# Optimization experiments

Hardware: AMD Instinct MI355X
Metric: run time of the kernel (lower is better)

## Reference

```python
import jax, jax.numpy as jnp
import numpy as np

EPS = 1e-7


def squash(s):
    # safe norm over last axis, keepdims
    norm = jnp.sqrt(jnp.sum(jnp.square(s), axis=-1, keepdims=True) + EPS)
    norm_sq = jnp.square(norm)
    return norm_sq / (1.0 + norm_sq) / norm * s


def setup_inputs() -> dict:
    key = jax.random.key(0)
    k1, k2 = jax.random.split(key)
    B, IN_CAPS, IN_DIM = 64, 2048, 16
    N_CAPS, CAP_DIM = 64, 16
    x = jax.random.normal(k1, (B, IN_CAPS, IN_DIM), dtype=jnp.float32)
    # glorot-uniform-ish init for W
    limit = (6.0 / (IN_DIM + N_CAPS * CAP_DIM)) ** 0.5
    W = jax.random.uniform(k2, (IN_CAPS, IN_DIM, N_CAPS * CAP_DIM),
                           minval=-limit, maxval=limit, dtype=jnp.float32)
    bias = jnp.zeros((N_CAPS, CAP_DIM), dtype=jnp.float32)
    return {"x": x, "W": W, "bias": bias}


def reference(x, W, bias):
    B, in_caps, in_dim = x.shape
    n_caps, cap_dim = bias.shape
    r_iters = 3
    # projection: [B, in_caps, n_caps*cap_dim] -> [B, in_caps, n_caps, cap_dim]
    u_hat = jnp.einsum('bij,ijk->bik', x, W).reshape(B, in_caps, n_caps, cap_dim)
    b = jnp.zeros((B, in_caps, n_caps, 1), dtype=u_hat.dtype)
    v = None
    for r in range(r_iters):
        c = jax.nn.softmax(b, axis=2)                       # route over class caps
        s = jnp.sum(u_hat * c, axis=1, keepdims=True)       # [B, 1, n_caps, cap_dim]
        s = s + bias
        v = squash(s)
        if r < r_iters - 1:
            agreement = jnp.sum(u_hat * v, axis=-1, keepdims=True)
            b = b + agreement
    return jnp.squeeze(v, axis=1)                           # [B, n_caps, cap_dim]
```

## Files before the change

### kernel.cpp

```cpp
#include <hip/hip_runtime.h>
#include <hip/hip_bf16.h>
#include <hip/hip_fp16.h>
#include <cstdio>

#define B_  64
#define I_  2048
#define J_  16
#define N_  64
#define D_  16
#define K_  1024

using short8 = __attribute__((ext_vector_type(8))) short;
using f32x16 = __attribute__((ext_vector_type(16))) float;

#if __has_builtin(__builtin_amdgcn_cvt_pk_u8_f32)
#define CVTPK_U8(f, sel, old) (unsigned)__builtin_amdgcn_cvt_pk_u8_f32((f), (sel), (old))
#else
__device__ __forceinline__ unsigned cvtpk_u8_sw(float f, unsigned sel, unsigned old) {
  unsigned b = (unsigned)(int)f & 0xffu;
  unsigned sh = sel * 8u;
  return (old & ~(0xffu << sh)) | (b << sh);
}
#define CVTPK_U8(f, sel, old) cvtpk_u8_sw((f), (sel), (old))
#endif

__device__ __forceinline__ short8 pack_bf16x8(float a0, float a1, float a2, float a3,
                                              float a4, float a5, float a6, float a7) {
  __hip_bfloat162 p0 = __float22bfloat162_rn(float2{a0, a1});
  __hip_bfloat162 p1 = __float22bfloat162_rn(float2{a2, a3});
  __hip_bfloat162 p2 = __float22bfloat162_rn(float2{a4, a5});
  __hip_bfloat162 p3 = __float22bfloat162_rn(float2{a6, a7});
  union { unsigned u[4]; short8 s; } cv;
  cv.u[0] = *(unsigned*)&p0; cv.u[1] = *(unsigned*)&p1;
  cv.u[2] = *(unsigned*)&p2; cv.u[3] = *(unsigned*)&p3;
  return cv.s;
}

__global__ __launch_bounds__(256, 5) void project_k(const float* __restrict__ x,
                                                    const float* __restrict__ W,
                                                    unsigned char* __restrict__ uh,
                                                    unsigned short* __restrict__ sc,
                                                    float* __restrict__ s_zero) {
  const int i  = blockIdx.x >> 2;
  const int ph = blockIdx.x & 3;
  const int t  = threadIdx.x;
  const int l  = t & 63;
  const int wv = t >> 6;
  const int h  = l >> 5;
  const int lr = l & 31;

  __shared__ unsigned       out_lds[64 * 65];
  __shared__ unsigned short sc_lds[64 * 20];

  if (blockIdx.x < 768) s_zero[blockIdx.x * 256 + t] = 0.f;

  short8 xfrag[2];
#pragma unroll
  for (int bt = 0; bt < 2; ++bt) {
    const float* xp = x + ((size_t)(bt * 32 + lr) * I_ + i) * J_ + h * 8;
    float4 f0 = *(const float4*)xp;
    float4 f1 = *(const float4*)(xp + 4);
    xfrag[bt] = pack_bf16x8(f0.x, f0.y, f0.z, f0.w, f1.x, f1.y, f1.z, f1.w);
  }

  const float* wbase = W + (size_t)i * (J_ * K_) + ph * 256;

#pragma unroll
  for (int kx = 0; kx < 2; ++kx) {
    const int kt = wv * 2 + kx;
    float wf[8];
#pragma unroll
    for (int e = 0; e < 8; ++e)
      wf[e] = wbase[(size_t)(h * 8 + e) * K_ + kt * 32 + lr];
    short8 afrag = pack_bf16x8(wf[0], wf[1], wf[2], wf[3], wf[4], wf[5], wf[6], wf[7]);

#pragma unroll
    for (int bt = 0; bt < 2; ++bt) {
      f32x16 acc = {0.f, 0.f, 0.f, 0.f, 0.f, 0.f, 0.f, 0.f,
                    0.f, 0.f, 0.f, 0.f, 0.f, 0.f, 0.f, 0.f};
      acc = __builtin_amdgcn_mfma_f32_32x32x16_bf16(afrag, xfrag[bt], acc, 0, 0, 0);
      const int b = bt * 32 + lr;

#define QCAP(C8, CS) do {                                                       \
      float ax = fabsf(acc[(C8) + 0]);                                          \
      ax = fmaxf(ax, fabsf(acc[(C8) + 1]));                                     \
      ax = fmaxf(ax, fabsf(acc[(C8) + 2]));                                     \
      ax = fmaxf(ax, fabsf(acc[(C8) + 3]));                                     \
      ax = fmaxf(ax, fabsf(acc[(C8) + 4]));                                     \
      ax = fmaxf(ax, fabsf(acc[(C8) + 5]));                                     \
      ax = fmaxf(ax, fabsf(acc[(C8) + 6]));                                     \
      ax = fmaxf(ax, fabsf(acc[(C8) + 7]));                                     \
      ax = fmaxf(ax, __shfl_xor(ax, 32));                                       \
      float inv = __fdividef(127.0f, fmaxf(ax, 1e-30f));                        \
      unsigned pk0 = CVTPK_U8(rintf(fmaf(acc[(C8) + 0], inv, 128.f)), 0u, 0u);  \
      pk0 = CVTPK_U8(rintf(fmaf(acc[(C8) + 1], inv, 128.f)), 1u, pk0);          \
      pk0 = CVTPK_U8(rintf(fmaf(acc[(C8) + 2], inv, 128.f)), 2u, pk0);          \
      pk0 = CVTPK_U8(rintf(fmaf(acc[(C8) + 3], inv, 128.f)), 3u, pk0);          \
      unsigned pk1 = CVTPK_U8(rintf(fmaf(acc[(C8) + 4], inv, 128.f)), 0u, 0u);  \
      pk1 = CVTPK_U8(rintf(fmaf(acc[(C8) + 5], inv, 128.f)), 1u, pk1);          \
      pk1 = CVTPK_U8(rintf(fmaf(acc[(C8) + 6], inv, 128.f)), 2u, pk1);          \
      pk1 = CVTPK_U8(rintf(fmaf(acc[(C8) + 7], inv, 128.f)), 3u, pk1);          \
      const int ibase = kt * 8 + (CS) * 4;                                      \
      out_lds[b * 65 + ibase + h]     = pk0;                                    \
      out_lds[b * 65 + ibase + 2 + h] = pk1;                                    \
      if (h == 0)                                                               \
        sc_lds[b * 20 + kt * 2 + (CS)] =                                        \
            __half_as_ushort(__float2half_rn(ax * (1.0f / 127.0f)));            \
    } while (0)

      QCAP(0, 0);
      QCAP(8, 1);
#undef QCAP
    }
  }
  __syncthreads();

  {
    const int c = t & 15;
#pragma unroll
    for (int it = 0; it < 4; ++it) {
      int bf = (t >> 4) + it * 16;
      const unsigned* rp = &out_lds[bf * 65 + c * 4];
      uint4 v;
      v.x = rp[0]; v.y = rp[1]; v.z = rp[2]; v.w = rp[3];
      *(uint4*)(uh + (size_t)bf * I_ * K_ + (size_t)i * K_ + ph * 256 + c * 16) = v;
    }
    int b2 = t >> 2, n4 = (t & 3) * 4;
    uint2 sv = *(const uint2*)&sc_lds[b2 * 20 + n4];
    *(uint2*)(sc + (size_t)b2 * I_ * N_ + (size_t)i * N_ + ph * 16 + n4) = sv;
  }
}

template <int MODE>
__global__ __launch_bounds__(256, 4) void route_k(const unsigned char* __restrict__ uh,
                                                  const unsigned short* __restrict__ sc,
                                                  const float* __restrict__ sa,
                                                  const float* __restrict__ sb,
                                                  const float* __restrict__ bias,
                                                  float* __restrict__ s_out) {
  const int t    = threadIdx.x;
  const int lane = t & 63;
  const int wv   = t >> 6;
  const int b    = blockIdx.x >> 4;
  const int iw   = ((blockIdx.x & 15) << 2) + wv;
  const int i0   = iw * 32;

  float vsum[16];
  float voff = 0.f;
  if (MODE >= 1) {
    float bs[16];
#pragma unroll
    for (int q = 0; q < 4; ++q) {
      float4 bb4 = *(const float4*)&bias[lane * 16 + q * 4];
      bs[q*4+0] = bb4.x; bs[q*4+1] = bb4.y; bs[q*4+2] = bb4.z; bs[q*4+3] = bb4.w;
    }
    {
      float va[16], nn = 0.f;
#pragma unroll
      for (int q = 0; q < 4; ++q) {
        float4 tmp = *(const float4*)&sa[(size_t)b * K_ + lane * 16 + q * 4];
        va[q*4+0] = tmp.x + bs[q*4+0]; va[q*4+1] = tmp.y + bs[q*4+1];
        va[q*4+2] = tmp.z + bs[q*4+2]; va[q*4+3] = tmp.w + bs[q*4+3];
      }
#pragma unroll
      for (int d = 0; d < 16; ++d) nn += va[d] * va[d];
      float n2 = nn + 1e-7f;
      float f = sqrtf(n2) / (1.0f + n2);
#pragma unroll
      for (int d = 0; d < 16; ++d) vsum[d] = va[d] * f;
    }
    if (MODE == 2) {
      float vb[16], nn = 0.f;
#pragma unroll
      for (int q = 0; q < 4; ++q) {
        float4 tmp = *(const float4*)&sb[(size_t)b * K_ + lane * 16 + q * 4];
        vb[q*4+0] = tmp.x + bs[q*4+0]; vb[q*4+1] = tmp.y + bs[q*4+1];
        vb[q*4+2] = tmp.z + bs[q*4+2]; vb[q*4+3] = tmp.w + bs[q*4+3];
      }
#pragma unroll
      for (int d = 0; d < 16; ++d) nn += vb[d] * vb[d];
      float n2 = nn + 1e-7f;
      float f = sqrtf(n2) / (1.0f + n2);
#pragma unroll
      for (int d = 0; d < 16; ++d) vsum[d] += vb[d] * f;
    }
    float tv = 0.f;
#pragma unroll
    for (int d = 0; d < 16; ++d) tv += vsum[d];
    voff = 128.0f * tv;
  }

  constexpr int IPW = 32;
  constexpr int PF  = 4;

  const unsigned char*  base = uh + (size_t)b * I_ * K_ + lane * 16;
  const unsigned short* scb  = sc + (size_t)b * I_ * N_ + lane;

  uint4 dbuf[PF];
  unsigned short hbuf[PF];
#pragma unroll
  for (int p = 0; p < PF; ++p) {
    int ip = (i0 + p) & (I_ - 1);
    dbuf[p] = *(const uint4*)(base + (size_t)ip * K_);
    hbuf[p] = scb[(size_t)ip * N_];
  }

  float s_loc[16];
#pragma unroll
  for (int d = 0; d < 16; ++d) s_loc[d] = 0.f;
  float csum = 0.f;

  for (int ii = 0; ii < IPW; ii += PF) {
#pragma unroll
    for (int p = 0; p < PF; ++p) {
      float scale = __half2float(__ushort_as_half(hbuf[p]));
      float u[16];
      {
        unsigned wd;
        wd = dbuf[p].x;
        u[0]  = (float)(wd & 0xffu);         u[1]  = (float)((wd >> 8) & 0xffu);
        u[2]  = (float)((wd >> 16) & 0xffu); u[3]  = (float)(wd >> 24);
        wd = dbuf[p].y;
        u[4]  = (float)(wd & 0xffu);         u[5]  = (float)((wd >> 8) & 0xffu);
        u[6]  = (float)((wd >> 16) & 0xffu); u[7]  = (float)(wd >> 24);
        wd = dbuf[p].z;
        u[8]  = (float)(wd & 0xffu);         u[9]  = (float)((wd >> 8) & 0xffu);
        u[10] = (float)((wd >> 16) & 0xffu); u[11] = (float)(wd >> 24);
        wd = dbuf[p].w;
        u[12] = (float)(wd & 0xffu);         u[13] = (float)((wd >> 8) & 0xffu);
        u[14] = (float)((wd >> 16) & 0xffu); u[15] = (float)(wd >> 24);
      }

      int ip = (i0 + ii + p + PF) & (I_ - 1);
      dbuf[p] = *(const uint4*)(base + (size_t)ip * K_);
      hbuf[p] = scb[(size_t)ip * N_];

      if (MODE == 0) {
#pragma unroll
        for (int d = 0; d < 16; ++d) s_loc[d] = fmaf(scale, u[d], s_loc[d]);
        csum += scale;
      } else {
        float dot = 0.f;
#pragma unroll
        for (int d = 0; d < 16; ++d) dot = fmaf(u[d], vsum[d], dot);
        float bl = scale * (dot - voff);
        float m = bl;
        m = fmaxf(m, __shfl_xor(m, 1));
        m = fmaxf(m, __shfl_xor(m, 2));
        m = fmaxf(m, __shfl_xor(m, 4));
        m = fmaxf(m, __shfl_xor(m, 8));
        m = fmaxf(m, __shfl_xor(m, 16));
        m = fmaxf(m, __shfl_xor(m, 32));
        float e = __expf(bl - m);
        float ss = e;
        ss += __shfl_xor(ss, 1);
        ss += __shfl_xor(ss, 2);
        ss += __shfl_xor(ss, 4);
        ss += __shfl_xor(ss, 8);
        ss += __shfl_xor(ss, 16);
        ss += __shfl_xor(ss, 32);
        float cs = __fdividef(e, ss) * scale;
#pragma unroll
        for (int d = 0; d < 16; ++d) s_loc[d] = fmaf(cs, u[d], s_loc[d]);
        csum += cs;
      }
    }
  }

#pragma unroll
  for (int d = 0; d < 16; ++d) s_loc[d] -= 128.0f * csum;
  if (MODE == 0) {
#pragma unroll
    for (int d = 0; d < 16; ++d) s_loc[d] *= (1.0f / 64.0f);
  }

  __shared__ float sred[4][64 * 17];
#pragma unroll
  for (int d = 0; d < 16; ++d) sred[wv][lane * 17 + d] = s_loc[d];
  __syncthreads();
#pragma unroll
  for (int e = 0; e < 4; ++e) {
    int idx = t * 4 + e;
    int n = idx >> 4, d = idx & 15;
    float val = sred[0][n*17+d] + sred[1][n*17+d] + sred[2][n*17+d] + sred[3][n*17+d];
    atomicAdd(&s_out[(size_t)b * K_ + idx], val);
  }
}

__global__ __launch_bounds__(256) void squash_k(const float* __restrict__ s_in,
                                                const float* __restrict__ bias,
                                                float* __restrict__ v_out) {
  const int b = blockIdx.x, t = threadIdx.x, k0 = t * 4;
  float4 s = *(const float4*)&s_in[b * K_ + k0];
  float4 bb = *(const float4*)&bias[k0];
  s.x += bb.x; s.y += bb.y; s.z += bb.z; s.w += bb.w;
  float p = s.x * s.x + s.y * s.y + s.z * s.z + s.w * s.w;
  p += __shfl_xor(p, 1);
  p += __shfl_xor(p, 2);
  float n2 = p + 1e-7f;
  float nrm = sqrtf(n2);
  float f = nrm / (1.0f + n2);
  float4 o = {s.x * f, s.y * f, s.z * f, s.w * f};
  *(float4*)&v_out[b * K_ + k0] = o;
}

extern "C" void kernel_launch(void* const* d_in, const int* in_sizes, int n_in,
                              void* d_out, int out_size, void* d_ws, size_t ws_size,
                              hipStream_t stream) {
  const float* x    = (const float*)d_in[0];
  const float* W    = (const float*)d_in[1];
  const float* bias = (const float*)d_in[2];
  float* out = (float*)d_out;

  char* ws = (char*)d_ws;
  size_t off = 0;
  unsigned char*  uh = (unsigned char*)(ws + off);  off += (size_t)B_ * I_ * K_;
  unsigned short* sc = (unsigned short*)(ws + off); off += (size_t)B_ * I_ * N_ * 2;
  float* s0 = (float*)(ws + off); off += (size_t)B_ * K_ * 4;
  float* s1 = (float*)(ws + off); off += (size_t)B_ * K_ * 4;
  float* s2 = (float*)(ws + off); off += (size_t)B_ * K_ * 4;

  if (ws_size < off)
    fprintf(stderr, "ClassCapsule: ws_size=%zu < needed=%zu — expect corruption\n", ws_size, off);

  project_k<<<dim3(I_ * 4), dim3(256), 0, stream>>>(x, W, uh, sc, s0);

  route_k<0><<<dim3(1024), dim3(256), 0, stream>>>(uh, sc, nullptr, nullptr, bias, s0);
  route_k<1><<<dim3(1024), dim3(256), 0, stream>>>(uh, sc, s0, nullptr, bias, s1);
  route_k<2><<<dim3(1024), dim3(256), 0, stream>>>(uh, sc, s0, s1, bias, s2);
  squash_k<<<dim3(B_), dim3(256), 0, stream>>>(s2, bias, out);
}
```

Baseline: 171.2 us.

## Merge projection phases into one block with register-prefetched W chunks

Each project_k block now handles all four 256-column phases of one input capsule instead of launching four blocks per capsule. The x fragments are loaded and packed once per block, and the next phase's W values are prefetched into registers while the current phase's MFMA, quantisation and stores run. The goal is less redundant x loading and per-block overhead, and hiding W load latency. In exchange the grid is four times smaller, the occupancy hint drops from 5 to 3, register use grows, and each phase adds two block-wide barriers.

```diff
diff --git a/kernel.cpp b/kernel.cpp
--- a/kernel.cpp
+++ b/kernel.cpp
@@ -36,13 +36,12 @@
   return cv.s;
 }
 
-__global__ __launch_bounds__(256, 5) void project_k(const float* __restrict__ x,
+__global__ __launch_bounds__(256, 3) void project_k(const float* __restrict__ x,
                                                     const float* __restrict__ W,
                                                     unsigned char* __restrict__ uh,
                                                     unsigned short* __restrict__ sc,
                                                     float* __restrict__ s_zero) {
-  const int i  = blockIdx.x >> 2;
-  const int ph = blockIdx.x & 3;
+  const int i  = blockIdx.x;
   const int t  = threadIdx.x;
   const int l  = t & 63;
   const int wv = t >> 6;
@@ -63,71 +62,90 @@
     xfrag[bt] = pack_bf16x8(f0.x, f0.y, f0.z, f0.w, f1.x, f1.y, f1.z, f1.w);
   }
 
-  const float* wbase = W + (size_t)i * (J_ * K_) + ph * 256;
-
-#pragma unroll
-  for (int kx = 0; kx < 2; ++kx) {
-    const int kt = wv * 2 + kx;
-    float wf[8];
+  const float* wrow = W + (size_t)i * (J_ * K_);
+
+  float wcur[16], wnxt[16];
+#pragma unroll
+  for (int kx = 0; kx < 2; ++kx)
 #pragma unroll
     for (int e = 0; e < 8; ++e)
-      wf[e] = wbase[(size_t)(h * 8 + e) * K_ + kt * 32 + lr];
-    short8 afrag = pack_bf16x8(wf[0], wf[1], wf[2], wf[3], wf[4], wf[5], wf[6], wf[7]);
-
-#pragma unroll
-    for (int bt = 0; bt < 2; ++bt) {
-      f32x16 acc = {0.f, 0.f, 0.f, 0.f, 0.f, 0.f, 0.f, 0.f,
-                    0.f, 0.f, 0.f, 0.f, 0.f, 0.f, 0.f, 0.f};
-      acc = __builtin_amdgcn_mfma_f32_32x32x16_bf16(afrag, xfrag[bt], acc, 0, 0, 0);
-      const int b = bt * 32 + lr;
+      wcur[kx * 8 + e] = wrow[(size_t)(h * 8 + e) * K_ + (wv * 2 + kx) * 32 + lr];
+
+#pragma unroll
+  for (int ph = 0; ph < 4; ++ph) {
+    if (ph < 3) {
+#pragma unroll
+      for (int kx = 0; kx < 2; ++kx)
+#pragma unroll
+        for (int e = 0; e < 8; ++e)
+          wnxt[kx * 8 + e] =
+              wrow[(size_t)(h * 8 + e) * K_ + (ph + 1) * 256 + (wv * 2 + kx) * 32 + lr];
+    }
+
+#pragma unroll
+    for (int kx = 0; kx < 2; ++kx) {
+      const int kt = wv * 2 + kx;
+      short8 afrag = pack_bf16x8(wcur[kx*8+0], wcur[kx*8+1], wcur[kx*8+2], wcur[kx*8+3],
+                                 wcur[kx*8+4], wcur[kx*8+5], wcur[kx*8+6], wcur[kx*8+7]);
+#pragma unroll
+      for (int bt = 0; bt < 2; ++bt) {
+        f32x16 acc = {0.f, 0.f, 0.f, 0.f, 0.f, 0.f, 0.f, 0.f,
+                      0.f, 0.f, 0.f, 0.f, 0.f, 0.f, 0.f, 0.f};
+        acc = __builtin_amdgcn_mfma_f32_32x32x16_bf16(afrag, xfrag[bt], acc, 0, 0, 0);
+        const int b = bt * 32 + lr;
 
 #define QCAP(C8, CS) do {                                                       \
-      float ax = fabsf(acc[(C8) + 0]);                                          \
-      ax = fmaxf(ax, fabsf(acc[(C8) + 1]));                                     \
-      ax = fmaxf(ax, fabsf(acc[(C8) + 2]));                                     \
-      ax = fmaxf(ax, fabsf(acc[(C8) + 3]));                                     \
-      ax = fmaxf(ax, fabsf(acc[(C8) + 4]));                                     \
-      ax = fmaxf(ax, fabsf(acc[(C8) + 5]));                                     \
-      ax = fmaxf(ax, fabsf(acc[(C8) + 6]));                                     \
-      ax = fmaxf(ax, fabsf(acc[(C8) + 7]));                                     \
-      ax = fmaxf(ax, __shfl_xor(ax, 32));                                       \
-      float inv = __fdividef(127.0f, fmaxf(ax, 1e-30f));                        \
-      unsigned pk0 = CVTPK_U8(rintf(fmaf(acc[(C8) + 0], inv, 128.f)), 0u, 0u);  \
-      pk0 = CVTPK_U8(rintf(fmaf(acc[(C8) + 1], inv, 128.f)), 1u, pk0);          \
-      pk0 = CVTPK_U8(rintf(fmaf(acc[(C8) + 2], inv, 128.f)), 2u, pk0);          \
-      pk0 = CVTPK_U8(rintf(fmaf(acc[(C8) + 3], inv, 128.f)), 3u, pk0);          \
-      unsigned pk1 = CVTPK_U8(rintf(fmaf(acc[(C8) + 4], inv, 128.f)), 0u, 0u);  \
-      pk1 = CVTPK_U8(rintf(fmaf(acc[(C8) + 5], inv, 128.f)), 1u, pk1);          \
-      pk1 = CVTPK_U8(rintf(fmaf(acc[(C8) + 6], inv, 128.f)), 2u, pk1);          \
-      pk1 = CVTPK_U8(rintf(fmaf(acc[(C8) + 7], inv, 128.f)), 3u, pk1);          \
-      const int ibase = kt * 8 + (CS) * 4;                                      \
-      out_lds[b * 65 + ibase + h]     = pk0;                                    \
-      out_lds[b * 65 + ibase + 2 + h] = pk1;                                    \
-      if (h == 0)                                                               \
-        sc_lds[b * 20 + kt * 2 + (CS)] =                                        \
-            __half_as_ushort(__float2half_rn(ax * (1.0f / 127.0f)));            \
-    } while (0)
-
-      QCAP(0, 0);
-      QCAP(8, 1);
+        float ax = fabsf(acc[(C8) + 0]);                                        \
+        ax = fmaxf(ax, fabsf(acc[(C8) + 1]));                                   \
+        ax = fmaxf(ax, fabsf(acc[(C8) + 2]));                                   \
+        ax = fmaxf(ax, fabsf(acc[(C8) + 3]));                                   \
+        ax = fmaxf(ax, fabsf(acc[(C8) + 4]));                                   \
+        ax = fmaxf(ax, fabsf(acc[(C8) + 5]));                                   \
+        ax = fmaxf(ax, fabsf(acc[(C8) + 6]));                                   \
+        ax = fmaxf(ax, fabsf(acc[(C8) + 7]));                                   \
+        ax = fmaxf(ax, __shfl_xor(ax, 32));                                     \
+        float inv = __fdividef(127.0f, fmaxf(ax, 1e-30f));                      \
+        unsigned pk0 = CVTPK_U8(rintf(fmaf(acc[(C8) + 0], inv, 128.f)), 0u, 0u);\
+        pk0 = CVTPK_U8(rintf(fmaf(acc[(C8) + 1], inv, 128.f)), 1u, pk0);        \
+        pk0 = CVTPK_U8(rintf(fmaf(acc[(C8) + 2], inv, 128.f)), 2u, pk0);        \
+        pk0 = CVTPK_U8(rintf(fmaf(acc[(C8) + 3], inv, 128.f)), 3u, pk0);        \
+        unsigned pk1 = CVTPK_U8(rintf(fmaf(acc[(C8) + 4], inv, 128.f)), 0u, 0u);\
+        pk1 = CVTPK_U8(rintf(fmaf(acc[(C8) + 5], inv, 128.f)), 1u, pk1);        \
+        pk1 = CVTPK_U8(rintf(fmaf(acc[(C8) + 6], inv, 128.f)), 2u, pk1);        \
+        pk1 = CVTPK_U8(rintf(fmaf(acc[(C8) + 7], inv, 128.f)), 3u, pk1);        \
+        const int ibase = kt * 8 + (CS) * 4;                                    \
+        out_lds[b * 65 + ibase + h]     = pk0;                                  \
+        out_lds[b * 65 + ibase + 2 + h] = pk1;                                  \
+        if (h == 0)                                                             \
+          sc_lds[b * 20 + kt * 2 + (CS)] =                                      \
+              __half_as_ushort(__float2half_rn(ax * (1.0f / 127.0f)));          \
+      } while (0)
+
+        QCAP(0, 0);
+        QCAP(8, 1);
 #undef QCAP
-    }
-  }
-  __syncthreads();
-
-  {
-    const int c = t & 15;
-#pragma unroll
-    for (int it = 0; it < 4; ++it) {
-      int bf = (t >> 4) + it * 16;
-      const unsigned* rp = &out_lds[bf * 65 + c * 4];
-      uint4 v;
-      v.x = rp[0]; v.y = rp[1]; v.z = rp[2]; v.w = rp[3];
-      *(uint4*)(uh + (size_t)bf * I_ * K_ + (size_t)i * K_ + ph * 256 + c * 16) = v;
-    }
-    int b2 = t >> 2, n4 = (t & 3) * 4;
-    uint2 sv = *(const uint2*)&sc_lds[b2 * 20 + n4];
-    *(uint2*)(sc + (size_t)b2 * I_ * N_ + (size_t)i * N_ + ph * 16 + n4) = sv;
+      }
+    }
+    __syncthreads();
+
+    {
+      const int c = t & 15;
+#pragma unroll
+      for (int it = 0; it < 4; ++it) {
+        int bf = (t >> 4) + it * 16;
+        const unsigned* rp = &out_lds[bf * 65 + c * 4];
+        uint4 v;
+        v.x = rp[0]; v.y = rp[1]; v.z = rp[2]; v.w = rp[3];
+        *(uint4*)(uh + (size_t)bf * I_ * K_ + (size_t)i * K_ + ph * 256 + c * 16) = v;
+      }
+      int b2 = t >> 2, n4 = (t & 3) * 4;
+      uint2 sv = *(const uint2*)&sc_lds[b2 * 20 + n4];
+      *(uint2*)(sc + (size_t)b2 * I_ * N_ + (size_t)i * N_ + ph * 16 + n4) = sv;
+    }
+    __syncthreads();
+
+#pragma unroll
+    for (int p = 0; p < 16; ++p) wcur[p] = wnxt[p];
   }
 }
 
@@ -323,7 +341,7 @@
   if (ws_size < off)
     fprintf(stderr, "ClassCapsule: ws_size=%zu < needed=%zu — expect corruption\n", ws_size, off);
 
-  project_k<<<dim3(I_ * 4), dim3(256), 0, stream>>>(x, W, uh, sc, s0);
+  project_k<<<dim3(I_), dim3(256), 0, stream>>>(x, W, uh, sc, s0);
 
   route_k<0><<<dim3(1024), dim3(256), 0, stream>>>(uh, sc, nullptr, nullptr, bias, s0);
   route_k<1><<<dim3(1024), dim3(256), 0, stream>>>(uh, sc, s0, nullptr, bias, s1);
```

New measurement: 160.3 us. 6.3% less time.
